# Optimization experiments

Measured on AMD Instinct MI355X. Metric: run time of the kernel, lower is better.

The kernel has to match this reference:

```python
import jax, jax.numpy as jnp
import numpy as np

TEMPERATURE = 0.07
MARGIN = 0.2
EPS = 1e-8  # matches torch F.cosine_similarity eps


def _cosine_matrix(a, b):
    # a: (N, D), b: (M, D) -> (N, M) pairwise cosine similarity
    an = a / jnp.clip(jnp.linalg.norm(a, axis=-1, keepdims=True), EPS)
    bn = b / jnp.clip(jnp.linalg.norm(b, axis=-1, keepdims=True), EPS)
    return an @ bn.T


def setup_inputs() -> dict:
    key = jax.random.key(0)
    k1, k2, k3 = jax.random.split(key, 3)
    return {
        "step_embeddings": jax.random.normal(k1, (8192, 1024), dtype=jnp.float32),
        "modal_embeddings": jax.random.normal(k2, (4096, 1024), dtype=jnp.float32),
        "negative_modal_embeddings": jax.random.normal(k3, (4096, 1024), dtype=jnp.float32),
    }


def reference(step_embeddings, modal_embeddings, negative_modal_embeddings):
    # --- step-modal alignment (max cosine sim per step, averaged) ---
    S = _cosine_matrix(step_embeddings, modal_embeddings)        # (N, M)
    per_step = S.max(axis=1)                                      # (N,)
    alignment = per_step.mean()

    # --- attention-weighted alignment (use_attention=True) ---
    logits = (step_embeddings @ modal_embeddings.T) / TEMPERATURE  # (N, M)
    attention = jax.nn.softmax(logits, axis=1)
    weighted_alignment = (S * attention).sum(axis=1).mean()

    # --- contrastive coherence against negatives ---
    Sn = _cosine_matrix(step_embeddings, negative_modal_embeddings)
    negative_alignment = Sn.max(axis=1).mean()
    positive_alignment = alignment
    contrastive_score = positive_alignment - negative_alignment
    margin_score = jax.nn.relu(contrastive_score - MARGIN)

    # --- per-step coherence (same max-cosine per step) ---
    min_step_coherence = per_step.min()

    # overall uses weighted_alignment (attention on), mixed with contrastive
    overall = 0.7 * weighted_alignment + 0.3 * contrastive_score

    return (alignment, weighted_alignment, attention, contrastive_score,
            margin_score, positive_alignment, negative_alignment,
            per_step, min_step_coherence, overall)
```

## Files before the change

kernel.cpp:

```cpp
#include <hip/hip_runtime.h>
#include <cmath>


#define WAVE 64

typedef __bf16 bf16x8_t __attribute__((ext_vector_type(8)));
typedef __bf16 bf16x4_t __attribute__((ext_vector_type(4)));
typedef float f32x4_t __attribute__((ext_vector_type(4)));

__device__ __forceinline__ float wave_reduce_sum(float v) {
#pragma unroll
    for (int o = 32; o > 0; o >>= 1) v += __shfl_down(v, o, WAVE);
    return v;
}
__device__ __forceinline__ float wave_reduce_max(float v) {
#pragma unroll
    for (int o = 32; o > 0; o >>= 1) v = fmaxf(v, __shfl_down(v, o, WAVE));
    return v;
}
__device__ __forceinline__ float wave_reduce_min(float v) {
#pragma unroll
    for (int o = 32; o > 0; o >>= 1) v = fminf(v, __shfl_down(v, o, WAVE));
    return v;
}

__device__ __forceinline__ unsigned enc_f(float f) {
    unsigned u = __float_as_uint(f);
    return (u & 0x80000000u) ? ~u : (u | 0x80000000u);
}
__device__ __forceinline__ float dec_f(unsigned e) {
    unsigned u = (e & 0x80000000u) ? (e & 0x7fffffffu) : ~e;
    return __uint_as_float(u);
}

__global__ __launch_bounds__(256)
void convert_norms_kernel(const float* __restrict__ step,
                          const float* __restrict__ modal,
                          const float* __restrict__ negs,
                          char* __restrict__ arena,
                          float* __restrict__ ina, float* __restrict__ inb,
                          float* __restrict__ inn,
                          unsigned* __restrict__ negmax_u, int N, int M) {
    const int tid = threadIdx.x, lane = tid & 63, wv = tid >> 6;
    const int b = blockIdx.x * 4 + wv;
    const float* src;
    if (b < N)          src = step  + (size_t)b * 1024;
    else if (b < N + M) src = modal + (size_t)(b - N) * 1024;
    else                src = negs  + (size_t)(b - N - M) * 1024;

    char* cb = arena + (((size_t)(b >> 2)) << 14) + ((size_t)(b & 3) << 11) + 8192;
    float s = 0.0f;
#pragma unroll
    for (int q = 0; q < 4; q++) {
        const int idx = lane + q * 64;
        const float4 v = ((const float4*)src)[idx];
        bf16x4_t o;
        o[0] = (__bf16)v.x; o[1] = (__bf16)v.y;
        o[2] = (__bf16)v.z; o[3] = (__bf16)v.w;
        *(bf16x4_t*)(cb + (size_t)idx * 8) = o;
        s += v.x * v.x + v.y * v.y + v.z * v.z + v.w * v.w;
    }
    s = wave_reduce_sum(s);
    if (lane == 0) {
        const float inv = 1.0f / fmaxf(sqrtf(s), 1e-8f);
        if (b < N)          { ina[b] = inv; negmax_u[b] = 0u; }
        else if (b < N + M) inb[b - N] = inv;
        else                inn[b - N - M] = inv;
    }
}

#define GLD16(g, l)                                                       \
    __builtin_amdgcn_global_load_lds(                                     \
        (const __attribute__((address_space(1))) void*)(g),               \
        (__attribute__((address_space(3))) void*)(l), 16, 0, 0)

#define BAR()   asm volatile("s_barrier" ::: "memory")
#define LGKM0() asm volatile("s_waitcnt lgkmcnt(0)" ::: "memory")
#define VMW(n)  asm volatile("s_waitcnt vmcnt(" #n ")" ::: "memory")

#define STAGE_A(Ab, kt)                                                   \
    _Pragma("unroll")                                                     \
    for (int h = 0; h < 2; h++)                                           \
    _Pragma("unroll")                                                     \
      for (int c = 0; c < 2; c++)                                         \
        GLD16(arena + srcA[h][c] + (size_t)(kt) * 128,                    \
              (Ab) + h * 8192 + c * 4096 + w * 512);

#define STAGE_B(Bb, kt)                                                   \
    _Pragma("unroll")                                                     \
    for (int h = 0; h < 2; h++)                                           \
    _Pragma("unroll")                                                     \
      for (int c = 0; c < 2; c++)                                         \
        GLD16(arena + srcB[h][c] + (size_t)(kt) * 128,                    \
              (Bb) + h * 8192 + c * 4096 + w * 512);

#define READ_A(g, Ab)                                                     \
    _Pragma("unroll")                                                     \
    for (int ii = 0; ii < 4; ii++)                                        \
    _Pragma("unroll")                                                     \
      for (int kk = 0; kk < 2; kk++)                                      \
        af[ii][kk] = *(const bf16x8_t*)&(Ab)[arow0 + (g) * 4096 +         \
                                             ii * 1024 + koff[kk]];

#define READ_B(j0, dst, Bb)                                               \
    _Pragma("unroll")                                                     \
    for (int jj = 0; jj < 2; jj++)                                        \
    _Pragma("unroll")                                                     \
      for (int kk = 0; kk < 2; kk++)                                      \
        dst[jj][kk] = *(const bf16x8_t*)&(Bb)[brow0 + ((j0) + jj) * 1024 +\
                                              koff[kk]];

#define READ_B01(Bb) READ_B(0, bf01, Bb)
#define READ_B23(Bb) READ_B(2, bf23, Bb)

#define MFMA_Q(i0, j0, bsrc)                                              \
    __builtin_amdgcn_s_setprio(1);                                        \
    _Pragma("unroll")                                                     \
    for (int kk = 0; kk < 2; kk++)                                        \
    _Pragma("unroll")                                                     \
      for (int ii = 0; ii < 4; ii++)                                      \
      _Pragma("unroll")                                                   \
        for (int jj = 0; jj < 2; jj++)                                    \
          acc[(i0) + ii][(j0) + jj] =                                     \
              __builtin_amdgcn_mfma_f32_16x16x32_bf16(                    \
                  af[ii][kk], bsrc[jj][kk], acc[(i0) + ii][(j0) + jj],    \
                  0, 0, 0);                                               \
    __builtin_amdgcn_s_setprio(0);

#define TILE(Ac, Bc, An, Bn, ktpre, pre, rd)                              \
    LGKM0();                     \
    MFMA_Q(0, 0, bf01);                                                   \
    READ_B23(Bc);                           \
    LGKM0();                                                              \
    MFMA_Q(0, 2, bf23);                                                   \
    READ_A(1, Ac);          \
    BAR();                        \
    if (pre) { STAGE_B(Bc, ktpre); }                                      \
    LGKM0();                                             \
    MFMA_Q(4, 0, bf01);                                                   \
    BAR();                        \
    if (pre) { STAGE_A(Ac, ktpre); }                                      \
    MFMA_Q(4, 2, bf23);                                                   \
    if (rd) {                                                             \
        if (pre) { VMW(8); } else { VMW(0); }                             \
        BAR();                      \
        READ_A(0, An);           \
        READ_B01(Bn);                                                     \
    }

__global__ __launch_bounds__(512, 2)
void gemm_fused_kernel(char* __restrict__ arena, int N, int M,
                       const float* __restrict__ inv_nn,
                       unsigned* __restrict__ negmax_u) {
    __shared__ __bf16 As[2][256 * 64];
    __shared__ __bf16 Bs[2][256 * 64];

    const int lin = blockIdx.x;
    const int xcd = lin & 7;
    const int j   = lin >> 3;
    const int r   = j >> 5;
    const int u   = j & 31;
    const int bm = ((xcd << 2) + (u & 3)) << 8;
    const int bn = ((r << 3) + (u >> 2)) << 8;

    const int t = threadIdx.x, w = t >> 6, lane = t & 63;
    const int lane16 = lane & 15, lq = lane >> 4;
    const int wm = w >> 2, wn = w & 3;

    const int l3 = lane >> 3, ol = lane & 7;
    const int og = ol ^ l3;
    unsigned srcA[2][2], srcB[2][2];
#pragma unroll
    for (int h = 0; h < 2; h++)
#pragma unroll
      for (int c = 0; c < 2; c++) {
        const int ga = bm + h * 128 + c * 64 + w * 8 + l3;
        srcA[h][c] = ((unsigned)(ga >> 2) << 14) + ((unsigned)(ga & 3) << 11)
                     + 8192u + (unsigned)og * 16u;
        const int gb = N + bn + h * 128 + c * 64 + w * 8 + l3;
        srcB[h][c] = ((unsigned)(gb >> 2) << 14) + ((unsigned)(gb & 3) << 11)
                     + 8192u + (unsigned)og * 16u;
      }

    const int sxr = lane16 & 7;
    int koff[2];
#pragma unroll
    for (int kk = 0; kk < 2; kk++) koff[kk] = ((lq + 4 * kk) ^ sxr) * 8;
    const int arow0 = wm * 8192 + lane16 * 64;
    const int brow0 = wn * 4096 + lane16 * 64;

    f32x4_t acc[8][4];
#pragma unroll
    for (int i = 0; i < 8; i++)
#pragma unroll
      for (int j2 = 0; j2 < 4; j2++) acc[i][j2] = (f32x4_t){0.f, 0.f, 0.f, 0.f};

    bf16x8_t af[4][2], bf01[2][2], bf23[2][2];

    __bf16* const A0 = As[0]; __bf16* const A1 = As[1];
    __bf16* const B0 = Bs[0]; __bf16* const B1 = Bs[1];

    STAGE_A(A0, 0); STAGE_B(B0, 0);
    STAGE_A(A1, 1); STAGE_B(B1, 1);
    VMW(8);
    BAR();
    READ_A(0, A0);
    READ_B01(B0);

    for (int it = 0; it < 8; ++it) {
        const int pre = (it < 7);
        const int k2 = 2 * it + 2, k3 = 2 * it + 3;
        TILE(A0, B0, A1, B1, k2, pre, 1)
        TILE(A1, B1, A0, B0, k3, pre, pre)
    }

    if (bn < M) {
#pragma unroll
        for (int i = 0; i < 8; i++) {
#pragma unroll
            for (int rr = 0; rr < 4; rr++) {
                const int grow = bm + wm * 128 + i * 16 + lq * 4 + rr;
                __bf16* dst = (__bf16*)(arena + ((size_t)grow << 14)) +
                              bn + wn * 64 + lane16;
#pragma unroll
                for (int jj = 0; jj < 4; jj++)
                    dst[jj * 16] = (__bf16)acc[i][jj][rr];
            }
        }
    } else {
        float invn[4];
#pragma unroll
        for (int jj = 0; jj < 4; jj++)
            invn[jj] = inv_nn[(bn - M) + wn * 64 + jj * 16 + lane16];
#pragma unroll
        for (int i = 0; i < 8; i++) {
#pragma unroll
            for (int rr = 0; rr < 4; rr++) {
                float v = acc[i][0][rr] * invn[0];
                v = fmaxf(v, acc[i][1][rr] * invn[1]);
                v = fmaxf(v, acc[i][2][rr] * invn[2]);
                v = fmaxf(v, acc[i][3][rr] * invn[3]);
#pragma unroll
                for (int o = 8; o > 0; o >>= 1)
                    v = fmaxf(v, __shfl_xor(v, o, WAVE));
                if (lane16 == 0)
                    atomicMax(&negmax_u[bm + wm * 128 + i * 16 + lq * 4 + rr],
                              enc_f(v));
            }
        }
    }
}

#define CUT 2.0f
#define MAXCAND 64
#define SROWS 4

__global__ __launch_bounds__(256)
void softmax_fix_kernel(char* __restrict__ arena, const float* __restrict__ step,
                        const float* __restrict__ modal,
                        const float* __restrict__ ina, const float* __restrict__ inb,
                        float* __restrict__ perstep, float* __restrict__ wout,
                        float* __restrict__ attn) {
    const int row0 = blockIdx.x * SROWS, tid = threadIdx.x;
    const int lane = tid & 63, wv = tid >> 6;

    __shared__ float srow_s[1024];
    __shared__ float red[8];
    __shared__ float bcast[2];
    __shared__ int   cand[MAXCAND];
    __shared__ float exact[MAXCAND];
    __shared__ int   cnt;

    float invn[16];
#pragma unroll
    for (int g = 0; g < 4; g++) {
        const float4 x = *(const float4*)(inb + g * 1024 + tid * 4);
        invn[g * 4 + 0] = x.x; invn[g * 4 + 1] = x.y;
        invn[g * 4 + 2] = x.z; invn[g * 4 + 3] = x.w;
    }
    const float invT = 1.0f / 0.07f;

    for (int rr = 0; rr < SROWS; rr++) {
        const int row = row0 + rr;
        if (tid == 0) cnt = 0;
        ((float4*)srow_s)[tid] = ((const float4*)(step + (size_t)row * 1024))[tid];

        const __bf16* gb = (const __bf16*)(arena + ((size_t)row << 14));
        float vals[16];
#pragma unroll
        for (int g = 0; g < 4; g++) {
            const bf16x4_t v = *(const bf16x4_t*)(gb + g * 1024 + tid * 4);
            vals[g * 4 + 0] = (float)v[0]; vals[g * 4 + 1] = (float)v[1];
            vals[g * 4 + 2] = (float)v[2]; vals[g * 4 + 3] = (float)v[3];
        }

        float dmax = -3.4e38f;
#pragma unroll
        for (int j = 0; j < 16; j++) dmax = fmaxf(dmax, vals[j]);
        float wm = wave_reduce_max(dmax);
        if (lane == 0) red[wv] = wm;
        __syncthreads();
        if (tid == 0) bcast[0] = fmaxf(fmaxf(red[0], red[1]),
                                       fmaxf(red[2], red[3]));
        __syncthreads();
        const float m0 = bcast[0];

        const float thr = m0 - CUT;
#pragma unroll
        for (int g = 0; g < 4; g++)
#pragma unroll
            for (int u = 0; u < 4; u++) {
                if (vals[g * 4 + u] >= thr) {
                    const int pos = atomicAdd(&cnt, 1);
                    if (pos < MAXCAND) cand[pos] = g * 1024 + tid * 4 + u;
                }
            }
        __syncthreads();
        const int nc = min(cnt, MAXCAND);

        for (int i = wv; i < nc; i += 4) {
            const float* mrow = modal + (size_t)cand[i] * 1024;
            float p = 0.0f;
#pragma unroll
            for (int q = 0; q < 16; q++) {
                const int idx = lane + q * 64;
                p = fmaf(srow_s[idx], mrow[idx], p);
            }
            p = wave_reduce_sum(p);
            if (lane == 0) exact[i] = p;
        }
        __syncthreads();

        for (int i = 0; i < nc; i++) {
            const int c = cand[i];
            if (((c & 1023) >> 2) == tid) vals[(c >> 10) * 4 + (c & 3)] = exact[i];
        }
        if (tid == 0) {
            float mx = -3.4e38f;
            for (int i = 0; i < nc; i++) mx = fmaxf(mx, exact[i]);
            bcast[0] = mx;
        }
        __syncthreads();
        const float mlog = bcast[0] * invT;

        float lsum = 0.0f, cmax = -3.4e38f;
#pragma unroll
        for (int j = 0; j < 16; j++) {
            lsum += __expf(vals[j] * invT - mlog);
            cmax = fmaxf(cmax, vals[j] * invn[j]);
        }
        lsum = wave_reduce_sum(lsum);
        float wc = wave_reduce_max(cmax);
        if (lane == 0) { red[wv] = lsum; red[4 + wv] = wc; }
        __syncthreads();
        if (tid == 0) {
            bcast[0] = red[0] + red[1] + red[2] + red[3];
            bcast[1] = fmaxf(fmaxf(red[4], red[5]), fmaxf(red[6], red[7]));
        }
        __syncthreads();
        const float invZ = 1.0f / bcast[0];
        const float cmaxAll = bcast[1];

        float* arow = attn + (size_t)row * 4096;
        float wacc = 0.0f;
#pragma unroll
        for (int g = 0; g < 4; g++) {
            float4 o;
            const float a0 = __expf(vals[g * 4 + 0] * invT - mlog) * invZ;
            const float a1 = __expf(vals[g * 4 + 1] * invT - mlog) * invZ;
            const float a2 = __expf(vals[g * 4 + 2] * invT - mlog) * invZ;
            const float a3 = __expf(vals[g * 4 + 3] * invT - mlog) * invZ;
            o.x = a0; o.y = a1; o.z = a2; o.w = a3;
            *(float4*)(arow + g * 1024 + tid * 4) = o;
            wacc += a0 * vals[g * 4 + 0] * invn[g * 4 + 0];
            wacc += a1 * vals[g * 4 + 1] * invn[g * 4 + 1];
            wacc += a2 * vals[g * 4 + 2] * invn[g * 4 + 2];
            wacc += a3 * vals[g * 4 + 3] * invn[g * 4 + 3];
        }
        wacc = wave_reduce_sum(wacc);
        if (lane == 0) red[wv] = wacc;
        __syncthreads();
        if (tid == 0) {
            const float inv_na = ina[row];
            perstep[row] = cmaxAll * inv_na;
            wout[row] = (red[0] + red[1] + red[2] + red[3]) * inv_na;
        }
        __syncthreads();
    }
}

__global__ __launch_bounds__(1024)
void finalize_kernel(const float* __restrict__ perstep, const float* __restrict__ w,
                     const unsigned* __restrict__ negmax_u,
                     const float* __restrict__ ina, float* __restrict__ out,
                     int N, size_t NM) {
    float s_a = 0.0f, s_w = 0.0f, s_n = 0.0f, mn = 3.4e38f;
    for (int i = threadIdx.x; i < N; i += 1024) {
        const float p = perstep[i];
        s_a += p;
        s_w += w[i];
        s_n += dec_f(negmax_u[i]) * ina[i];
        mn = fminf(mn, p);
    }
    s_a = wave_reduce_sum(s_a);
    s_w = wave_reduce_sum(s_w);
    s_n = wave_reduce_sum(s_n);
    mn  = wave_reduce_min(mn);
    __shared__ float ra[16], rw[16], rn[16], rm[16];
    const int lane = threadIdx.x & 63, wv = threadIdx.x >> 6;
    if (lane == 0) { ra[wv] = s_a; rw[wv] = s_w; rn[wv] = s_n; rm[wv] = mn; }
    __syncthreads();
    if (threadIdx.x == 0) {
        float ta = 0, tw = 0, tn = 0, tm = 3.4e38f;
#pragma unroll
        for (int i = 0; i < 16; i++) {
            ta += ra[i]; tw += rw[i]; tn += rn[i]; tm = fminf(tm, rm[i]);
        }
        const float inv = 1.0f / (float)N;
        const float alignment = ta * inv;
        const float weighted  = tw * inv;
        const float neg       = tn * inv;
        const float contrast  = alignment - neg;
        const float margin    = fmaxf(contrast - 0.2f, 0.0f);
        const float overall   = 0.7f * weighted + 0.3f * contrast;
        out[0] = alignment;
        out[1] = weighted;
        float* p = out + 2 + NM;
        p[0] = contrast;
        p[1] = margin;
        p[2] = alignment;
        p[3] = neg;
        p[4 + N] = tm;
        p[5 + N] = overall;
    }
}

extern "C" void kernel_launch(void* const* d_in, const int* in_sizes, int n_in,
                              void* d_out, int out_size, void* d_ws, size_t ws_size,
                              hipStream_t stream) {
    const float* step  = (const float*)d_in[0];
    const float* modal = (const float*)d_in[1];
    const float* negs  = (const float*)d_in[2];
    float* out = (float*)d_out;

    const int K = 1024;
    const int N = in_sizes[0] / K;
    const int M = in_sizes[1] / K;
    const size_t NM = (size_t)N * (size_t)M;

    float* ina        = (float*)d_ws;
    float* inb        = ina + N;
    float* inn        = inb + M;
    unsigned* negmax  = (unsigned*)(inn + M);
    float* wsum       = (float*)(negmax + N);

    char* arena    = (char*)d_out + 16;
    float* attn    = out + 2;
    float* perstep = out + 2 + NM + 4;

    convert_norms_kernel<<<(N + 2 * M) / 4, 256, 0, stream>>>(
        step, modal, negs, arena, ina, inb, inn, negmax, N, M);

    const int nblocks = (N >> 8) * ((2 * M) >> 8);
    gemm_fused_kernel<<<nblocks, 512, 0, stream>>>(arena, N, M, inn, negmax);

    softmax_fix_kernel<<<N / SROWS, 256, 0, stream>>>(arena, step, modal, ina,
                                                      inb, perstep, wsum, attn);

    finalize_kernel<<<1, 1024, 0, stream>>>(perstep, wsum, negmax, ina, out, N, NM);
}
```

Before: 356.1 us.

## Shrink GEMM tile to 256x128 with K=32 steps and simpler pipeline

Changes the fused GEMM block tile from 256x256 with K=64 stages to 256x128 with K=32 stages, using 8 waves in a 4x2 layout with a 4x4 accumulator grid each. LDS use drops, so launch bounds now ask for 4 blocks per CU. The interleaved quarter-MFMA schedule is replaced by a simpler one-MFMA-batch-per-K-step double-buffered loop, and the grid doubles. The aim is higher occupancy and better latency hiding, at the cost of less data reuse per block, more barriers per unit of work, and a less finely interleaved schedule.

```diff
diff --git a/kernel.cpp b/kernel.cpp
--- a/kernel.cpp
+++ b/kernel.cpp
@@ -78,148 +78,107 @@
 #define LGKM0() asm volatile("s_waitcnt lgkmcnt(0)" ::: "memory")
 #define VMW(n)  asm volatile("s_waitcnt vmcnt(" #n ")" ::: "memory")
 
-#define STAGE_A(Ab, kt)                                                   \
+#define STAGE_AB(Ab, Bb, kt)                                              \
     _Pragma("unroll")                                                     \
     for (int h = 0; h < 2; h++)                                           \
+        GLD16(arena + srcA[h] + (size_t)(kt) * 64,                        \
+              (Ab) + h * 4096 + w * 512);                                 \
+    GLD16(arena + srcB + (size_t)(kt) * 64, (Bb) + w * 512);
+
+#define READ_FRAGS(Ab, Bb)                                                \
     _Pragma("unroll")                                                     \
-      for (int c = 0; c < 2; c++)                                         \
-        GLD16(arena + srcA[h][c] + (size_t)(kt) * 128,                    \
-              (Ab) + h * 8192 + c * 4096 + w * 512);
-
-#define STAGE_B(Bb, kt)                                                   \
+    for (int ii = 0; ii < 4; ii++)                                        \
+        af[ii] = *(const bf16x8_t*)&(Ab)[aoff + ii * 512];                \
     _Pragma("unroll")                                                     \
-    for (int h = 0; h < 2; h++)                                           \
-    _Pragma("unroll")                                                     \
-      for (int c = 0; c < 2; c++)                                         \
-        GLD16(arena + srcB[h][c] + (size_t)(kt) * 128,                    \
-              (Bb) + h * 8192 + c * 4096 + w * 512);
-
-#define READ_A(g, Ab)                                                     \
+    for (int jj = 0; jj < 4; jj++)                                        \
+        bf[jj] = *(const bf16x8_t*)&(Bb)[boff + jj * 512];
+
+#define MFMA_ALL()                                                        \
+    __builtin_amdgcn_s_setprio(1);                                        \
     _Pragma("unroll")                                                     \
     for (int ii = 0; ii < 4; ii++)                                        \
     _Pragma("unroll")                                                     \
-      for (int kk = 0; kk < 2; kk++)                                      \
-        af[ii][kk] = *(const bf16x8_t*)&(Ab)[arow0 + (g) * 4096 +         \
-                                             ii * 1024 + koff[kk]];
-
-#define READ_B(j0, dst, Bb)                                               \
-    _Pragma("unroll")                                                     \
-    for (int jj = 0; jj < 2; jj++)                                        \
-    _Pragma("unroll")                                                     \
-      for (int kk = 0; kk < 2; kk++)                                      \
-        dst[jj][kk] = *(const bf16x8_t*)&(Bb)[brow0 + ((j0) + jj) * 1024 +\
-                                              koff[kk]];
-
-#define READ_B01(Bb) READ_B(0, bf01, Bb)
-#define READ_B23(Bb) READ_B(2, bf23, Bb)
-
-#define MFMA_Q(i0, j0, bsrc)                                              \
-    __builtin_amdgcn_s_setprio(1);                                        \
-    _Pragma("unroll")                                                     \
-    for (int kk = 0; kk < 2; kk++)                                        \
-    _Pragma("unroll")                                                     \
-      for (int ii = 0; ii < 4; ii++)                                      \
-      _Pragma("unroll")                                                   \
-        for (int jj = 0; jj < 2; jj++)                                    \
-          acc[(i0) + ii][(j0) + jj] =                                     \
-              __builtin_amdgcn_mfma_f32_16x16x32_bf16(                    \
-                  af[ii][kk], bsrc[jj][kk], acc[(i0) + ii][(j0) + jj],    \
-                  0, 0, 0);                                               \
+      for (int jj = 0; jj < 4; jj++)                                      \
+        acc[ii][jj] = __builtin_amdgcn_mfma_f32_16x16x32_bf16(            \
+            af[ii], bf[jj], acc[ii][jj], 0, 0, 0);                        \
     __builtin_amdgcn_s_setprio(0);
 
-#define TILE(Ac, Bc, An, Bn, ktpre, pre, rd)                              \
-    LGKM0();                     \
-    MFMA_Q(0, 0, bf01);                                                   \
-    READ_B23(Bc);                           \
-    LGKM0();                                                              \
-    MFMA_Q(0, 2, bf23);                                                   \
-    READ_A(1, Ac);          \
-    BAR();                        \
-    if (pre) { STAGE_B(Bc, ktpre); }                                      \
-    LGKM0();                                             \
-    MFMA_Q(4, 0, bf01);                                                   \
-    BAR();                        \
-    if (pre) { STAGE_A(Ac, ktpre); }                                      \
-    MFMA_Q(4, 2, bf23);                                                   \
-    if (rd) {                                                             \
-        if (pre) { VMW(8); } else { VMW(0); }                             \
-        BAR();                      \
-        READ_A(0, An);           \
-        READ_B01(Bn);                                                     \
-    }
-
-__global__ __launch_bounds__(512, 2)
+__global__ __launch_bounds__(512, 4)
 void gemm_fused_kernel(char* __restrict__ arena, int N, int M,
                        const float* __restrict__ inv_nn,
                        unsigned* __restrict__ negmax_u) {
-    __shared__ __bf16 As[2][256 * 64];
-    __shared__ __bf16 Bs[2][256 * 64];
+    __shared__ __bf16 As[2][256 * 32];
+    __shared__ __bf16 Bs[2][128 * 32];
 
     const int lin = blockIdx.x;
     const int xcd = lin & 7;
     const int j   = lin >> 3;
-    const int r   = j >> 5;
-    const int u   = j & 31;
+    const int r   = j >> 6;
+    const int u   = j & 63;
     const int bm = ((xcd << 2) + (u & 3)) << 8;
-    const int bn = ((r << 3) + (u >> 2)) << 8;
+    const int bn = ((r << 4) + (u >> 2)) << 7;
 
     const int t = threadIdx.x, w = t >> 6, lane = t & 63;
     const int lane16 = lane & 15, lq = lane >> 4;
-    const int wm = w >> 2, wn = w & 3;
-
-    const int l3 = lane >> 3, ol = lane & 7;
-    const int og = ol ^ l3;
-    unsigned srcA[2][2], srcB[2][2];
-#pragma unroll
-    for (int h = 0; h < 2; h++)
-#pragma unroll
-      for (int c = 0; c < 2; c++) {
-        const int ga = bm + h * 128 + c * 64 + w * 8 + l3;
-        srcA[h][c] = ((unsigned)(ga >> 2) << 14) + ((unsigned)(ga & 3) << 11)
-                     + 8192u + (unsigned)og * 16u;
-        const int gb = N + bn + h * 128 + c * 64 + w * 8 + l3;
-        srcB[h][c] = ((unsigned)(gb >> 2) << 14) + ((unsigned)(gb & 3) << 11)
-                     + 8192u + (unsigned)og * 16u;
-      }
-
-    const int sxr = lane16 & 7;
-    int koff[2];
-#pragma unroll
-    for (int kk = 0; kk < 2; kk++) koff[kk] = ((lq + 4 * kk) ^ sxr) * 8;
-    const int arow0 = wm * 8192 + lane16 * 64;
-    const int brow0 = wn * 4096 + lane16 * 64;
-
-    f32x4_t acc[8][4];
-#pragma unroll
-    for (int i = 0; i < 8; i++)
+    const int wm = w >> 1, wn = w & 1;
+
+    const int og = (lane & 3) ^ ((lane >> 3) & 3);
+    unsigned srcA[2], srcB;
+#pragma unroll
+    for (int h = 0; h < 2; h++) {
+        const int ga = bm + h * 128 + w * 16 + (lane >> 2);
+        srcA[h] = ((unsigned)(ga >> 2) << 14) + ((unsigned)(ga & 3) << 11)
+                  + 8192u + (unsigned)og * 16u;
+    }
+    {
+        const int gb = N + bn + w * 16 + (lane >> 2);
+        srcB = ((unsigned)(gb >> 2) << 14) + ((unsigned)(gb & 3) << 11)
+               + 8192u + (unsigned)og * 16u;
+    }
+
+    const int koff = (lq ^ ((lane16 >> 1) & 3)) * 8;
+    const int aoff = (wm * 64 + lane16) * 32 + koff;
+    const int boff = (wn * 64 + lane16) * 32 + koff;
+
+    f32x4_t acc[4][4];
+#pragma unroll
+    for (int i = 0; i < 4; i++)
 #pragma unroll
       for (int j2 = 0; j2 < 4; j2++) acc[i][j2] = (f32x4_t){0.f, 0.f, 0.f, 0.f};
 
-    bf16x8_t af[4][2], bf01[2][2], bf23[2][2];
+    bf16x8_t af[4], bf[4];
 
     __bf16* const A0 = As[0]; __bf16* const A1 = As[1];
     __bf16* const B0 = Bs[0]; __bf16* const B1 = Bs[1];
 
-    STAGE_A(A0, 0); STAGE_B(B0, 0);
-    STAGE_A(A1, 1); STAGE_B(B1, 1);
-    VMW(8);
+    STAGE_AB(A0, B0, 0);
+    STAGE_AB(A1, B1, 1);
+    VMW(3);
     BAR();
-    READ_A(0, A0);
-    READ_B01(B0);
-
-    for (int it = 0; it < 8; ++it) {
-        const int pre = (it < 7);
-        const int k2 = 2 * it + 2, k3 = 2 * it + 3;
-        TILE(A0, B0, A1, B1, k2, pre, 1)
-        TILE(A1, B1, A0, B0, k3, pre, pre)
+    READ_FRAGS(A0, B0);
+
+    for (int kt = 0; kt < 32; ++kt) {
+        const int pre = (kt < 30);
+        const int rd  = (kt < 31);
+        __bf16* const Ac = (kt & 1) ? A1 : A0;
+        __bf16* const Bc = (kt & 1) ? B1 : B0;
+        __bf16* const An = (kt & 1) ? A0 : A1;
+        __bf16* const Bn = (kt & 1) ? B0 : B1;
+        LGKM0();
+        MFMA_ALL();
+        BAR();
+        if (pre) { STAGE_AB(Ac, Bc, kt + 2); VMW(3); }
+        else     { VMW(0); }
+        BAR();
+        if (rd) { READ_FRAGS(An, Bn); }
     }
 
     if (bn < M) {
 #pragma unroll
-        for (int i = 0; i < 8; i++) {
+        for (int i = 0; i < 4; i++) {
 #pragma unroll
             for (int rr = 0; rr < 4; rr++) {
-                const int grow = bm + wm * 128 + i * 16 + lq * 4 + rr;
+                const int grow = bm + wm * 64 + i * 16 + lq * 4 + rr;
                 __bf16* dst = (__bf16*)(arena + ((size_t)grow << 14)) +
                               bn + wn * 64 + lane16;
 #pragma unroll
@@ -233,7 +192,7 @@
         for (int jj = 0; jj < 4; jj++)
             invn[jj] = inv_nn[(bn - M) + wn * 64 + jj * 16 + lane16];
 #pragma unroll
-        for (int i = 0; i < 8; i++) {
+        for (int i = 0; i < 4; i++) {
 #pragma unroll
             for (int rr = 0; rr < 4; rr++) {
                 float v = acc[i][0][rr] * invn[0];
@@ -244,7 +203,7 @@
                 for (int o = 8; o > 0; o >>= 1)
                     v = fmaxf(v, __shfl_xor(v, o, WAVE));
                 if (lane16 == 0)
-                    atomicMax(&negmax_u[bm + wm * 128 + i * 16 + lq * 4 + rr],
+                    atomicMax(&negmax_u[bm + wm * 64 + i * 16 + lq * 4 + rr],
                               enc_f(v));
             }
         }
@@ -461,7 +420,7 @@
     convert_norms_kernel<<<(N + 2 * M) / 4, 256, 0, stream>>>(
         step, modal, negs, arena, ina, inb, inn, negmax, N, M);
 
-    const int nblocks = (N >> 8) * ((2 * M) >> 8);
+    const int nblocks = (N >> 8) * ((2 * M) >> 7);
     gemm_fused_kernel<<<nblocks, 512, 0, stream>>>(arena, N, M, inn, negmax);
 
     softmax_fix_kernel<<<N / SROWS, 256, 0, stream>>>(arena, step, modal, ina,
```

New measurement: 387.9 us. +8.9%, slower.
